# Performance work log

Measured on AMD Instinct MI355X. Metric: run time of the kernel, lower is better.

## Reference

```python
import jax, jax.numpy as jnp
import numpy as np

B, C, H, W = 4, 64, 64, 64
CQK = C // 8


def setup_inputs() -> dict:
    key = jax.random.key(0)
    ks = jax.random.split(key, 4)
    x = jax.random.normal(ks[0], (B, C, H, W), dtype=jnp.float32)
    Wq = jax.random.normal(ks[1], (CQK, C), dtype=jnp.float32) * (1.0 / np.sqrt(C))
    bq = jnp.zeros((CQK,), dtype=jnp.float32)
    Wk = jax.random.normal(ks[2], (CQK, C), dtype=jnp.float32) * (1.0 / np.sqrt(C))
    bk = jnp.zeros((CQK,), dtype=jnp.float32)
    Wv = jax.random.normal(ks[3], (C, C), dtype=jnp.float32) * (1.0 / np.sqrt(C))
    bv = jnp.zeros((C,), dtype=jnp.float32)
    gamma = jnp.ones((1,), dtype=jnp.float32)
    return {"x": x, "Wq": Wq, "bq": bq, "Wk": Wk, "bk": bk,
            "Wv": Wv, "bv": bv, "gamma": gamma}


def reference(x, Wq, bq, Wk, bk, Wv, bv, gamma):
    b, c, h, w = x.shape
    n = h * w
    xf = x.reshape(b, c, n)                      # [B, C, N]
    # 1x1 convs == per-pixel linear over channels
    q = jnp.einsum('oc,bcn->bon', Wq, xf) + bq[:, None]   # [B, C/8, N]
    k = jnp.einsum('oc,bcn->bon', Wk, xf) + bk[:, None]   # [B, C/8, N]
    v = jnp.einsum('oc,bcn->bon', Wv, xf) + bv[:, None]   # [B, C, N]
    # attention_map[b,i,j] = <q[:, i], k[:, j]>; softmax over j
    attn = jax.nn.softmax(jnp.einsum('bci,bcj->bij', q, k), axis=-1)  # [B, N, N]
    # out[b,c,i] = sum_j v[b,c,j] * attn[b,i,j]  (bmm(V, attn^T))
    out = jnp.einsum('bcj,bij->bci', v, attn).reshape(b, c, h, w)
    return gamma * out + x
```

## Files before the change

kernel.cpp:

```cpp
#include <hip/hip_runtime.h>
#include <hip/hip_bf16.h>
#include <math.h>

#define NPIX 4096

typedef __attribute__((ext_vector_type(8))) short s8;
typedef __attribute__((ext_vector_type(16))) float f16v;

typedef __attribute__((address_space(1))) const void glob_cv;
typedef __attribute__((address_space(3))) void lds_v;

static __device__ __forceinline__ unsigned packbf2(float a, float b) {
    union { __hip_bfloat162 h; unsigned u; } x;
    x.h = __float22bfloat162_rn(make_float2(a, b));
    return x.u;
}
static __device__ __forceinline__ float fexp2(float x) {
#if __has_builtin(__builtin_amdgcn_exp2f)
    return __builtin_amdgcn_exp2f(x);
#else
    return exp2f(x);
#endif
}

static __device__ __forceinline__ void gl_lds16(const unsigned short* g,
                                                unsigned short* l, int lane) {
#if __has_builtin(__builtin_amdgcn_global_load_lds)
    __builtin_amdgcn_global_load_lds((glob_cv*)g, (lds_v*)l, 16, 0, 0);
#else
    *(uint4*)(l + lane * 8) = *(const uint4*)g;
#endif
}

static __device__ __forceinline__ void lane_swap(unsigned a, unsigned b, int lh,
                                                 unsigned &x, unsigned &y) {
#if __has_builtin(__builtin_amdgcn_permlane32_swap)
    auto r = __builtin_amdgcn_permlane32_swap((int)a, (int)b, false, false);
    x = (unsigned)r[0];
    y = (unsigned)r[1];
#else
    unsigned sa = __shfl_xor(a, 32), sb = __shfl_xor(b, 32);
    x = lh ? sb : a;
    y = lh ? b : sa;
#endif
}

__global__ __launch_bounds__(512) void prep_kernel(
    const float* __restrict__ x,
    const float* __restrict__ Wq, const float* __restrict__ bq,
    const float* __restrict__ Wk, const float* __restrict__ bk,
    __hip_bfloat16* __restrict__ qbf, __hip_bfloat16* __restrict__ kbf,
    __hip_bfloat16* __restrict__ xbf)
{
    __shared__ float Xp[64][65];
    __shared__ unsigned short Qs[64][8];
    int t = threadIdx.x;
    int p = t & 63;
    int g = t >> 6;
    int bid = blockIdx.x;
    int og = bid & 1;
    int n0 = ((bid >> 1) & 63) << 6;
    int b  = bid >> 7;

    const float* xb = x + ((size_t)b << 18);
    __hip_bfloat16* xbb = xbf + ((size_t)b << 18);
#pragma unroll
    for (int u = 0; u < 8; ++u) {
        int c = g + (u << 3);
        float v = xb[((size_t)c << 12) + n0 + p];
        Xp[c][p] = v;
        if ((og == 0) ? (u < 4) : (u >= 4))
            xbb[((size_t)c << 12) + n0 + p] = __float2bfloat16(v);
    }
    __syncthreads();

    const float* W  = og ? Wk : Wq;
    const float* bb = og ? bk : bq;
    const float* wr = W + g * 64;
    float acc = bb[g];
#pragma unroll
    for (int c = 0; c < 64; ++c) acc = fmaf(wr[c], Xp[c][p], acc);
    if (!og) acc *= 1.4426950408889634f;

    union { __hip_bfloat16 h; unsigned short u; } cv;
    cv.h = __float2bfloat16(acc);
    Qs[p][g] = cv.u;
    __syncthreads();

    if (t < 64) {
        __hip_bfloat16* dst = (og ? kbf : qbf) + ((size_t)(b * NPIX + n0 + t) << 3);
        *(s8*)dst = *(const s8*)&Qs[t][0];
    }
}

__global__ __launch_bounds__(512, 4) void flash_fused_kernel(
    const __hip_bfloat16* __restrict__ qbf, const __hip_bfloat16* __restrict__ kbf,
    const __hip_bfloat16* __restrict__ xbf,
    const float* __restrict__ Wv, const float* __restrict__ bv,
    const float* __restrict__ x, const float* __restrict__ gamma,
    float* __restrict__ out)
{
    __shared__ __align__(16) char pool[65536];
    unsigned short* Xs0 = (unsigned short*)pool;
    unsigned short* Xs1 = Xs0 + 16384;

    int t = threadIdx.x;
    int w    = t >> 6;
    int lane = t & 63;
    int l32  = lane & 31;
    int lh   = lane >> 5;

    int b  = blockIdx.x >> 7;
    int i0 = (blockIdx.x & 127) << 5;

    const s8 zero8 = {0, 0, 0, 0, 0, 0, 0, 0};

    s8 qf;
    {
        s8 qv = *(const s8*)(qbf + ((size_t)(b * NPIX + i0 + l32) << 3));
        qf = (lh == 0) ? qv : zero8;
    }

    f16v acc[2];
    f16v zero16;
#pragma unroll
    for (int r = 0; r < 16; ++r) { acc[0][r] = 0.f; acc[1][r] = 0.f; zero16[r] = 0.f; }
    float lsum = 0.f;

    const __hip_bfloat16* kb = kbf + ((size_t)(b * NPIX) << 3);
    const unsigned short* xg = (const unsigned short*)xbf + ((size_t)b << 18);

    int rhalf = lane >> 5, gl = lane & 31;
    int offv[4];
#pragma unroll
    for (int u = 0; u < 4; ++u) {
        int r = (w << 3) + (u << 1) + rhalf;
        offv[u] = (r << 12) + ((gl ^ (r & 31)) << 3);
    }
    int g1o = ((4 * w + lh) ^ l32) << 3;
    int g2o = ((4 * w + lh + 2) ^ l32) << 3;
    int woff = w * 32 + l32;

#define STAGE(BUF, JT) do {                                                  \
        unsigned short* lb_ = (BUF) + (w << 11);                             \
        _Pragma("unroll")                                                    \
        for (int u_ = 0; u_ < 4; ++u_)                                       \
            gl_lds16(xg + offv[u_] + (JT) * 256, lb_ + (u_ << 9), lane);     \
    } while (0)

#define BODY(XSB, KF, JT) do {                                               \
        f16v sC = __builtin_amdgcn_mfma_f32_32x32x16_bf16(KF, qf, zero16, 0, 0, 0); \
        float e_[16];                                                        \
        _Pragma("unroll")                                                    \
        for (int r_ = 0; r_ < 16; ++r_) e_[r_] = fexp2(sC[r_]);              \
        _Pragma("unroll")                                                    \
        for (int r_ = 0; r_ < 16; ++r_) lsum += e_[r_];                      \
        unsigned P2[8];                                                      \
        _Pragma("unroll")                                                    \
        for (int s_ = 0; s_ < 8; ++s_) P2[s_] = packbf2(e_[2*s_], e_[2*s_+1]); \
        unsigned b00,b01,b02,b03,b10,b11,b12,b13;                            \
        lane_swap(P2[0], P2[2], lh, b00, b02);                               \
        lane_swap(P2[1], P2[3], lh, b01, b03);                               \
        lane_swap(P2[4], P2[6], lh, b10, b12);                               \
        lane_swap(P2[5], P2[7], lh, b11, b13);                               \
        union { unsigned u[4]; s8 v; } bf0, bf1;                             \
        bf0.u[0]=b00; bf0.u[1]=b01; bf0.u[2]=b02; bf0.u[3]=b03;              \
        bf1.u[0]=b10; bf1.u[1]=b11; bf1.u[2]=b12; bf1.u[3]=b13;              \
        _Pragma("unroll")                                                    \
        for (int cm_ = 0; cm_ < 2; ++cm_) {                                  \
            const unsigned short* xr_ = (XSB) + ((cm_ * 32 + l32) << 8);     \
            union { uint2 u2[2]; s8 v; } xu0, xu1;                           \
            xu0.u2[0] = *(const uint2*)(xr_ + g1o);                          \
            xu0.u2[1] = *(const uint2*)(xr_ + g1o + 4);                      \
            acc[cm_] = __builtin_amdgcn_mfma_f32_32x32x16_bf16(xu0.v, bf0.v, acc[cm_], 0, 0, 0); \
            xu1.u2[0] = *(const uint2*)(xr_ + g2o);                          \
            xu1.u2[1] = *(const uint2*)(xr_ + g2o + 4);                      \
            acc[cm_] = __builtin_amdgcn_mfma_f32_32x32x16_bf16(xu1.v, bf1.v, acc[cm_], 0, 0, 0); \
        }                                                                    \
        __syncthreads();                     \
        if ((JT) < 14) {                                                     \
            STAGE(XSB, (JT) + 2);                                            \
            KF = *(const s8*)(kb + ((size_t)(((JT) + 2) * 256 + woff) << 3)); \
        }                                                                    \
    } while (0)

    STAGE(Xs0, 0);
    STAGE(Xs1, 1);
    s8 kfA = *(const s8*)(kb + ((size_t)woff << 3));
    s8 kfB = *(const s8*)(kb + ((size_t)(256 + woff) << 3));
    __syncthreads();

    for (int jt = 0; jt < 16; jt += 2) {
        BODY(Xs0, kfA, jt);
        BODY(Xs1, kfB, jt + 1);
    }
#undef BODY
#undef STAGE

    float* OshA = (float*)pool;
    float* OshB = (float*)(pool + 8704);
    float* Linv = (float*)(pool + 17408);
    float* bvs  = (float*)(pool + 17536);
    float* Wvs  = (float*)(pool + 17792);
    float* Lsh  = (float*)(pool + 34176);

    lsum += __shfl_xor(lsum, 32);
    if (lh == 0) Lsh[w * 32 + l32] = lsum;

    float* Og = (w >> 2) ? OshB : OshA;
    for (int s = 0; s < 4; ++s) {
        __syncthreads();
        if ((w & 3) == s) {
#pragma unroll
            for (int cm = 0; cm < 2; ++cm)
#pragma unroll
                for (int r = 0; r < 16; ++r) {
                    int cc = cm * 32 + (r & 3) + 8 * (r >> 2) + 4 * lh;
                    float* p = Og + l32 * 68 + cc;
                    if (s == 0) *p = acc[cm][r];
                    else        *p += acc[cm][r];
                }
        }
    }
    __syncthreads();

    if (t < 32) {
        float lt = 0.f;
#pragma unroll
        for (int ww = 0; ww < 8; ++ww) lt += Lsh[ww * 32 + t];
        Linv[t] = 1.0f / lt;
    }
    if (t < 64) bvs[t] = bv[t];
    {
        const float4* wsrc = (const float4*)Wv;
        float4* wdst = (float4*)Wvs;
        wdst[t] = wsrc[t];
        wdst[t + 512] = wsrc[t + 512];
    }
    __syncthreads();

    {
        int i  = t & 31;
        int cg = t >> 5;
        float inv = Linv[i];
        float res[4] = {0.f, 0.f, 0.f, 0.f};
#pragma unroll 4
        for (int cb = 0; cb < 16; ++cb) {
            float4 oa = *(const float4*)(OshA + i * 68 + cb * 4);
            float4 ob = *(const float4*)(OshB + i * 68 + cb * 4);
            float4 o = make_float4(oa.x + ob.x, oa.y + ob.y, oa.z + ob.z, oa.w + ob.w);
#pragma unroll
            for (int k = 0; k < 4; ++k) {
                const float4 wv4 = *(const float4*)(Wvs + (cg * 4 + k) * 64 + cb * 4);
                res[k] = fmaf(wv4.x, o.x, fmaf(wv4.y, o.y, fmaf(wv4.z, o.z, fmaf(wv4.w, o.w, res[k]))));
            }
        }
        float g = gamma[0];
        const float* xr = x + ((size_t)b << 18) + i0;
        float* outp = out + ((size_t)b << 18) + i0;
#pragma unroll
        for (int k = 0; k < 4; ++k) {
            int cch = cg * 4 + k;
            float attn = fmaf(res[k], inv, bvs[cch]);
            size_t off = ((size_t)cch << 12) + i;
            outp[off] = fmaf(g, attn, xr[off]);
        }
    }
}

extern "C" void kernel_launch(void* const* d_in, const int* in_sizes, int n_in,
                              void* d_out, int out_size, void* d_ws, size_t ws_size,
                              hipStream_t stream) {
    const float* x     = (const float*)d_in[0];
    const float* Wq    = (const float*)d_in[1];
    const float* bq    = (const float*)d_in[2];
    const float* Wk    = (const float*)d_in[3];
    const float* bk    = (const float*)d_in[4];
    const float* Wv    = (const float*)d_in[5];
    const float* bv    = (const float*)d_in[6];
    const float* gamma = (const float*)d_in[7];
    float* out = (float*)d_out;

    __hip_bfloat16* qbf = (__hip_bfloat16*)d_ws;
    __hip_bfloat16* kbf = qbf + (size_t)4 * NPIX * 8;
    __hip_bfloat16* xbf = kbf + (size_t)4 * NPIX * 8;

    prep_kernel<<<512, 512, 0, stream>>>(x, Wq, bq, Wk, bk, qbf, kbf, xbf);
    flash_fused_kernel<<<512, 512, 0, stream>>>(qbf, kbf, xbf, Wv, bv, x, gamma, out);
}
```

Before: 101.2 us.

## Give each wave a private key range and LDS buffer, drop block barriers

Previously every wave loaded a shared slice of X into a block-wide double buffer and the block synchronized on every key tile. Now each wave owns a contiguous 512-key chunk and its own double-buffered LDS region, and staging is guarded with per-wave s_waitcnt vmcnt instead of __syncthreads. The LDS layout is re-swizzled so each X fragment is a single 16-byte read. This removes block-wide barriers from the main loop, at the cost of depending on hand-written vmcnt counts. A barrier is added before the epilogue reuses the pool.

Measured after the change: 102.6 us. No clear change (+1.3%).

```diff
diff --git a/kernel.cpp b/kernel.cpp
--- a/kernel.cpp
+++ b/kernel.cpp
@@ -101,8 +101,6 @@
     float* __restrict__ out)
 {
     __shared__ __align__(16) char pool[65536];
-    unsigned short* Xs0 = (unsigned short*)pool;
-    unsigned short* Xs1 = Xs0 + 16384;
 
     int t = threadIdx.x;
     int w    = t >> 6;
@@ -127,28 +125,37 @@
     for (int r = 0; r < 16; ++r) { acc[0][r] = 0.f; acc[1][r] = 0.f; zero16[r] = 0.f; }
     float lsum = 0.f;
 
-    const __hip_bfloat16* kb = kbf + ((size_t)(b * NPIX) << 3);
+    const __hip_bfloat16* kb = kbf + ((size_t)(b * NPIX) << 3) + ((size_t)(w << 9) << 3);
     const unsigned short* xg = (const unsigned short*)xbf + ((size_t)b << 18);
 
-    int rhalf = lane >> 5, gl = lane & 31;
-    int offv[4];
+    unsigned short* mybuf = (unsigned short*)pool + (w << 12);
+
+    int l2 = lane >> 2, lg = lane & 3;
+    int srcb[4];
 #pragma unroll
     for (int u = 0; u < 4; ++u) {
-        int r = (w << 3) + (u << 1) + rhalf;
-        offv[u] = (r << 12) + ((gl ^ (r & 31)) << 3);
-    }
-    int g1o = ((4 * w + lh) ^ l32) << 3;
-    int g2o = ((4 * w + lh + 2) ^ l32) << 3;
-    int woff = w * 32 + l32;
-
-#define STAGE(BUF, JT) do {                                                  \
-        unsigned short* lb_ = (BUF) + (w << 11);                             \
+        int row = (u << 4) + l2;
+        srcb[u] = (row << 12) + (w << 9) + ((lg ^ ((row >> 1) & 3)) << 3);
+    }
+    int sw = (l32 >> 1) & 3;
+    int o00 = (l32 << 5) + ((lh ^ sw) << 3);
+    int o01 = (l32 << 5) + (((2 + lh) ^ sw) << 3);
+    int o10 = ((32 + l32) << 5) + ((lh ^ sw) << 3);
+    int o11 = ((32 + l32) << 5) + (((2 + lh) ^ sw) << 3);
+
+#define STAGE(BO, N) do {                                                    \
+        unsigned short* lb_ = mybuf + (BO);                                  \
         _Pragma("unroll")                                                    \
         for (int u_ = 0; u_ < 4; ++u_)                                       \
-            gl_lds16(xg + offv[u_] + (JT) * 256, lb_ + (u_ << 9), lane);     \
+            gl_lds16(xg + srcb[u_] + ((N) << 5), lb_ + (u_ << 9), lane);     \
     } while (0)
 
-#define BODY(XSB, KF, JT) do {                                               \
+#define WAITN(N) do {                                                        \
+        asm volatile("s_waitcnt vmcnt(" #N ")" ::: "memory");                \
+        __builtin_amdgcn_sched_barrier(0);                                   \
+    } while (0)
+
+#define BODY(BO, KF) do {                                                    \
         f16v sC = __builtin_amdgcn_mfma_f32_32x32x16_bf16(KF, qf, zero16, 0, 0, 0); \
         float e_[16];                                                        \
         _Pragma("unroll")                                                    \
@@ -166,35 +173,39 @@
         union { unsigned u[4]; s8 v; } bf0, bf1;                             \
         bf0.u[0]=b00; bf0.u[1]=b01; bf0.u[2]=b02; bf0.u[3]=b03;              \
         bf1.u[0]=b10; bf1.u[1]=b11; bf1.u[2]=b12; bf1.u[3]=b13;              \
-        _Pragma("unroll")                                                    \
-        for (int cm_ = 0; cm_ < 2; ++cm_) {                                  \
-            const unsigned short* xr_ = (XSB) + ((cm_ * 32 + l32) << 8);     \
-            union { uint2 u2[2]; s8 v; } xu0, xu1;                           \
-            xu0.u2[0] = *(const uint2*)(xr_ + g1o);                          \
-            xu0.u2[1] = *(const uint2*)(xr_ + g1o + 4);                      \
-            acc[cm_] = __builtin_amdgcn_mfma_f32_32x32x16_bf16(xu0.v, bf0.v, acc[cm_], 0, 0, 0); \
-            xu1.u2[0] = *(const uint2*)(xr_ + g2o);                          \
-            xu1.u2[1] = *(const uint2*)(xr_ + g2o + 4);                      \
-            acc[cm_] = __builtin_amdgcn_mfma_f32_32x32x16_bf16(xu1.v, bf1.v, acc[cm_], 0, 0, 0); \
-        }                                                                    \
-        __syncthreads();                     \
-        if ((JT) < 14) {                                                     \
-            STAGE(XSB, (JT) + 2);                                            \
-            KF = *(const s8*)(kb + ((size_t)(((JT) + 2) * 256 + woff) << 3)); \
-        }                                                                    \
+        const unsigned short* xb_ = mybuf + (BO);                            \
+        s8 xa;                                                               \
+        xa = *(const s8*)(xb_ + o00);                                        \
+        acc[0] = __builtin_amdgcn_mfma_f32_32x32x16_bf16(xa, bf0.v, acc[0], 0, 0, 0); \
+        xa = *(const s8*)(xb_ + o01);                                        \
+        acc[0] = __builtin_amdgcn_mfma_f32_32x32x16_bf16(xa, bf1.v, acc[0], 0, 0, 0); \
+        xa = *(const s8*)(xb_ + o10);                                        \
+        acc[1] = __builtin_amdgcn_mfma_f32_32x32x16_bf16(xa, bf0.v, acc[1], 0, 0, 0); \
+        xa = *(const s8*)(xb_ + o11);                                        \
+        acc[1] = __builtin_amdgcn_mfma_f32_32x32x16_bf16(xa, bf1.v, acc[1], 0, 0, 0); \
     } while (0)
 
-    STAGE(Xs0, 0);
-    STAGE(Xs1, 1);
-    s8 kfA = *(const s8*)(kb + ((size_t)woff << 3));
-    s8 kfB = *(const s8*)(kb + ((size_t)(256 + woff) << 3));
-    __syncthreads();
-
-    for (int jt = 0; jt < 16; jt += 2) {
-        BODY(Xs0, kfA, jt);
-        BODY(Xs1, kfB, jt + 1);
-    }
+    STAGE(0, 0);
+    STAGE(2048, 1);
+    s8 kfA = *(const s8*)(kb + ((size_t)l32 << 3));
+    s8 kfB = *(const s8*)(kb + ((size_t)(32 + l32) << 3));
+
+    for (int n = 0; n < 14; n += 2) {
+        WAITN(4);
+        BODY(0, kfA);
+        STAGE(0, n + 2);
+        kfA = *(const s8*)(kb + ((size_t)(((n + 2) << 5) + l32) << 3));
+        WAITN(4);
+        BODY(2048, kfB);
+        STAGE(2048, n + 3);
+        kfB = *(const s8*)(kb + ((size_t)(((n + 3) << 5) + l32) << 3));
+    }
+    WAITN(4);
+    BODY(0, kfA);
+    WAITN(0);
+    BODY(2048, kfB);
 #undef BODY
+#undef WAITN
 #undef STAGE
 
     float* OshA = (float*)pool;
@@ -205,6 +216,7 @@
     float* Lsh  = (float*)(pool + 34176);
 
     lsum += __shfl_xor(lsum, 32);
+    __syncthreads();
     if (lh == 0) Lsh[w * 32 + l32] = lsum;
 
     float* Og = (w >> 2) ? OshB : OshA;
```
